# Kernel optimization log

Measured on AMD Instinct MI355X. Metric: run time of the kernel, lower is better.

Reference implementation:

```python
import jax, jax.numpy as jnp
import numpy as np

B, T, S, V, E, H, ENC, SUM = 256, 64, 256, 512, 512, 1024, 1024, 2048
DECODE_RANGE = 512  # current_decode_range == full vocab here


def setup_inputs() -> dict:
    key = jax.random.key(0)
    ks = jax.random.split(key, 16)
    r = lambda k, shape: jax.random.normal(k, shape, dtype=jnp.float32) * 0.02
    z = lambda n: jnp.zeros((n,), dtype=jnp.float32)
    return {
        "y": jax.random.randint(ks[0], (B, T), 0, V),
        "encoder_embed": jax.random.normal(ks[1], (B, S, ENC), dtype=jnp.float32),
        "encoder_summary": jax.random.normal(ks[2], (B, SUM), dtype=jnp.float32),
        "emb_table": r(ks[3], (V, E)),
        "W_init": r(ks[4], (4 * H, SUM)), "b_init": z(4 * H),
        "W_ci": r(ks[5], (E, E + ENC)), "b_ci": z(E),
        "Wih0": r(ks[6], (4 * H, E)), "Whh0": r(ks[7], (4 * H, H)),
        "bih0": z(4 * H), "bhh0": z(4 * H),
        "Wih1": r(ks[8], (4 * H, H)), "Whh1": r(ks[9], (4 * H, H)),
        "bih1": z(4 * H), "bhh1": z(4 * H),
        "Wq": r(ks[10], (ENC, 2 * H)), "bq": z(ENC),
        "Wco": r(ks[11], (H, ENC + H)), "bco": z(H),
        "Wout": r(ks[12], (V, H)), "bout": z(V),
    }


def _lstm_cell(x, h, c, Wih, Whh, bih, bhh):
    # PyTorch LSTM gate order: i, f, g, o
    g = x @ Wih.T + h @ Whh.T + bih + bhh
    i, f, gg, o = jnp.split(g, 4, axis=-1)
    c = jax.nn.sigmoid(f) * c + jax.nn.sigmoid(i) * jnp.tanh(gg)
    h = jax.nn.sigmoid(o) * jnp.tanh(c)
    return h, c


def reference(y, encoder_embed, encoder_summary, emb_table, W_init, b_init,
              W_ci, b_ci, Wih0, Whh0, bih0, bhh0, Wih1, Whh1, bih1, bhh1,
              Wq, bq, Wco, bco, Wout, bout):
    bs = y.shape[0]
    hdim = Whh0.shape[1]
    # decoder_init: Linear+Tanh -> view(B,2,2,H).permute(1,2,0,3) -> (h0, c0), each (layers=2, B, H)
    init = jnp.tanh(encoder_summary @ W_init.T + b_init).reshape(bs, 2, 2, hdim)
    init = jnp.transpose(init, (1, 2, 0, 3))
    h0, c0 = init[0], init[1]
    cross0 = jnp.zeros((bs, encoder_embed.shape[-1]), dtype=encoder_embed.dtype)

    def step(carry, tok):
        h, c, cross = carry  # h, c: (2, B, H); cross: (B, ENC)
        emb = emb_table[tok]  # (B, E)
        emb = jnp.tanh(jnp.concatenate([emb, cross], -1) @ W_ci.T + b_ci)
        h_l0, c_l0 = _lstm_cell(emb, h[0], c[0], Wih0, Whh0, bih0, bhh0)
        h_l1, c_l1 = _lstm_cell(h_l0, h[1], c[1], Wih1, Whh1, bih1, bhh1)
        # attention query from cat(h, c) of last layer
        q = jnp.tanh(jnp.concatenate([h_l1, c_l1], -1) @ Wq.T + bq)  # (B, ENC)
        attn = jax.nn.softmax(jnp.einsum('be,bse->bs', q, encoder_embed), axis=-1)
        cross = jnp.einsum('bs,bse->be', attn, encoder_embed)  # (B, ENC)
        lin = jnp.tanh(jnp.concatenate([h_l1, cross], -1) @ Wco.T + bco)
        logits = lin @ Wout.T + bout  # (B, V)
        tok_out = jnp.argmax(logits[:, :DECODE_RANGE], axis=-1)
        return (jnp.stack([h_l0, h_l1]), jnp.stack([c_l0, c_l1]), cross), (logits, tok_out)

    _, (logits, toks) = jax.lax.scan(step, (h0, c0, cross0), y.T)
    decoder_tokens = jnp.transpose(toks, (1, 0))           # (B, T)
    decoder_linears = jnp.transpose(logits, (1, 0, 2))     # (B, T, V)
    return decoder_tokens, decoder_linears
```

## Files before the change

### kernel.cpp

```cpp
#include <hip/hip_runtime.h>
#include <math.h>

#define BB   256
#define TT   64
#define SS   256
#define VV   512
#define EE   512
#define HH   1024
#define ENCE 1024
#define SUME 2048
#define NSP  8

typedef __attribute__((ext_vector_type(8))) _Float16 h8v;
typedef __attribute__((ext_vector_type(4))) float f4v;

__device__ __forceinline__ void split16(float x, _Float16& h, _Float16& l) {
    h = (_Float16)x;
    l = (_Float16)((x - (float)h) * 4096.0f);
}

__global__ __launch_bounds__(256) void gemm2(
    const float* __restrict__ A0, const float* __restrict__ W0, const int K0,
    const int lda0, const int ldw0,
    const float* __restrict__ A1, const float* __restrict__ W1, const int Ktot,
    const int lda1, const int ldw1,
    const float* __restrict__ b0, const float* __restrict__ b1,
    float* __restrict__ C, const int ldc, const int act)
{
    __shared__ float As[16][68];
    __shared__ float Ws[16][68];

    const int tid = threadIdx.x;
    const int n0  = blockIdx.x * 64;
    const int m0  = blockIdx.y * 64;
    const int lr  = tid >> 2;
    const int lc  = (tid & 3) << 2;
    const int tx  = tid & 15;
    const int ty  = tid >> 4;

    float acc[4][4] = {{0.f}};

    for (int k0 = 0; k0 < Ktot; k0 += 16) {
        const float* A; const float* W; int lda, ldw, kk;
        if (k0 < K0) { A = A0; W = W0; lda = lda0; ldw = ldw0; kk = k0; }
        else         { A = A1; W = W1; lda = lda1; ldw = ldw1; kk = k0 - K0; }

        const float4 av = *(const float4*)(A + (size_t)(m0 + lr) * lda + kk + lc);
        const float4 wv = *(const float4*)(W + (size_t)(n0 + lr) * ldw + kk + lc);

        __syncthreads();
        As[lc + 0][lr] = av.x; As[lc + 1][lr] = av.y;
        As[lc + 2][lr] = av.z; As[lc + 3][lr] = av.w;
        Ws[lc + 0][lr] = wv.x; Ws[lc + 1][lr] = wv.y;
        Ws[lc + 2][lr] = wv.z; Ws[lc + 3][lr] = wv.w;
        __syncthreads();

        #pragma unroll
        for (int p = 0; p < 16; ++p) {
            const float4 a4 = *(const float4*)&As[p][ty * 4];
            const float4 w4 = *(const float4*)&Ws[p][tx * 4];
            acc[0][0] += a4.x * w4.x; acc[0][1] += a4.x * w4.y;
            acc[0][2] += a4.x * w4.z; acc[0][3] += a4.x * w4.w;
            acc[1][0] += a4.y * w4.x; acc[1][1] += a4.y * w4.y;
            acc[1][2] += a4.y * w4.z; acc[1][3] += a4.y * w4.w;
            acc[2][0] += a4.z * w4.x; acc[2][1] += a4.z * w4.y;
            acc[2][2] += a4.z * w4.z; acc[2][3] += a4.z * w4.w;
            acc[3][0] += a4.w * w4.x; acc[3][1] += a4.w * w4.y;
            acc[3][2] += a4.w * w4.z; acc[3][3] += a4.w * w4.w;
        }
    }

    float bias[4];
    #pragma unroll
    for (int j = 0; j < 4; ++j) {
        const int n = n0 + tx * 4 + j;
        bias[j] = b0[n] + (b1 ? b1[n] : 0.f);
    }
    #pragma unroll
    for (int i = 0; i < 4; ++i) {
        const int m = m0 + ty * 4 + i;
        #pragma unroll
        for (int j = 0; j < 4; ++j) {
            float v = acc[i][j] + bias[j];
            if (act) v = tanhf(v);
            C[(size_t)m * ldc + n0 + tx * 4 + j] = v;
        }
    }
}

__global__ void lstm_gate(const float* __restrict__ g,
                          float* __restrict__ h, float* __restrict__ c)
{
    const int i = blockIdx.x * blockDim.x + threadIdx.x;
    if (i >= BB * HH) return;
    const int b = i / HH, k = i % HH;
    const float* gb = g + (size_t)b * 4 * HH;
    const float gi = gb[k];
    const float gf = gb[HH + k];
    const float gg = gb[2 * HH + k];
    const float go = gb[3 * HH + k];
    const float si = 1.f / (1.f + expf(-gi));
    const float sf = 1.f / (1.f + expf(-gf));
    const float so = 1.f / (1.f + expf(-go));
    const float cn = sf * c[i] + si * tanhf(gg);
    c[i] = cn;
    h[i] = so * tanhf(cn);
}

__global__ __launch_bounds__(256) void attn_kernel(
    const float* __restrict__ q, const float* __restrict__ enc,
    float* __restrict__ cross)
{
    const int b = blockIdx.x, tid = threadIdx.x;
    __shared__ float qs[ENCE];
    __shared__ float sc[SS];
    __shared__ float red[256];

    const float* qb = q + (size_t)b * ENCE;
    const float* eb = enc + (size_t)b * SS * ENCE;

    for (int e = tid; e < ENCE; e += 256) qs[e] = qb[e];
    __syncthreads();

    {
        const float* row = eb + (size_t)tid * ENCE;
        float a = 0.f;
        for (int e = 0; e < ENCE; e += 4) {
            const float4 ev = *(const float4*)&row[e];
            a += ev.x * qs[e] + ev.y * qs[e + 1] + ev.z * qs[e + 2] + ev.w * qs[e + 3];
        }
        sc[tid] = a;
    }
    __syncthreads();

    red[tid] = sc[tid];
    __syncthreads();
    for (int off = 128; off > 0; off >>= 1) {
        if (tid < off) red[tid] = fmaxf(red[tid], red[tid + off]);
        __syncthreads();
    }
    const float mx = red[0];
    __syncthreads();
    const float ex = expf(sc[tid] - mx);
    red[tid] = ex;
    __syncthreads();
    for (int off = 128; off > 0; off >>= 1) {
        if (tid < off) red[tid] += red[tid + off];
        __syncthreads();
    }
    const float inv = 1.f / red[0];
    __syncthreads();
    sc[tid] = ex * inv;
    __syncthreads();

    float4 acc = {0.f, 0.f, 0.f, 0.f};
    const int e0 = tid * 4;
    for (int s = 0; s < SS; ++s) {
        const float w = sc[s];
        const float4 ev = *(const float4*)&eb[(size_t)s * ENCE + e0];
        acc.x += w * ev.x; acc.y += w * ev.y; acc.z += w * ev.z; acc.w += w * ev.w;
    }
    *(float4*)&cross[(size_t)b * ENCE + e0] = acc;
}

__global__ __launch_bounds__(256) void attn_part_k(
    const float* __restrict__ qpart, const float* __restrict__ bq,
    const float* __restrict__ enc,
    float* __restrict__ po, float* __restrict__ pm, float* __restrict__ pl)
{
    const int sp = blockIdx.x, b = blockIdx.y, tid = threadIdx.x;
    __shared__ float qs[ENCE];
    __shared__ float es[4 * ENCE];
    __shared__ float sc[4];

    {
        const int n = tid * 4;
        float4 s = *(const float4*)&bq[n];
        #pragma unroll
        for (int p = 0; p < 8; ++p) {
            const float4 v = *(const float4*)&qpart[
                (size_t)p * BB * ENCE + (size_t)b * ENCE + n];
            s.x += v.x; s.y += v.y; s.z += v.z; s.w += v.w;
        }
        qs[n]     = tanhf(s.x);
        qs[n + 1] = tanhf(s.y);
        qs[n + 2] = tanhf(s.z);
        qs[n + 3] = tanhf(s.w);
    }

    const float* eb = enc + (size_t)b * SS * ENCE + (size_t)sp * 32 * ENCE;

    float4 r0, r1, r2, r3;
    auto ldchunk = [&](int ch) {
        const float* src = eb + (size_t)ch * 4 * ENCE + tid * 4;
        r0 = *(const float4*)(src);
        r1 = *(const float4*)(src + ENCE);
        r2 = *(const float4*)(src + 2 * ENCE);
        r3 = *(const float4*)(src + 3 * ENCE);
    };
    ldchunk(0);
    __syncthreads();

    const int row  = tid >> 6;
    const int lane = tid & 63;
    const int e0   = tid * 4;

    float m = -INFINITY, l = 0.f;
    float4 o = {0.f, 0.f, 0.f, 0.f};

    for (int ch = 0; ch < 8; ++ch) {
        *(float4*)&es[tid * 4]            = r0;
        *(float4*)&es[tid * 4 + ENCE]     = r1;
        *(float4*)&es[tid * 4 + 2 * ENCE] = r2;
        *(float4*)&es[tid * 4 + 3 * ENCE] = r3;
        __syncthreads();

        if (ch + 1 < 8) ldchunk(ch + 1);

        {
            float a = 0.f;
            const float* er = &es[row * ENCE];
            #pragma unroll
            for (int j = 0; j < 4; ++j) {
                const int e = lane * 4 + j * 256;
                const float4 ev = *(const float4*)&er[e];
                const float4 qv = *(const float4*)&qs[e];
                a += ev.x * qv.x + ev.y * qv.y + ev.z * qv.z + ev.w * qv.w;
            }
            a += __shfl_xor(a, 1);
            a += __shfl_xor(a, 2);
            a += __shfl_xor(a, 4);
            a += __shfl_xor(a, 8);
            a += __shfl_xor(a, 16);
            a += __shfl_xor(a, 32);
            if (lane == 0) sc[row] = a;
        }
        __syncthreads();

        {
            const float cm = fmaxf(fmaxf(sc[0], sc[1]), fmaxf(sc[2], sc[3]));
            const float mn = fmaxf(m, cm);
            const float scale = expf(m - mn);
            o.x *= scale; o.y *= scale; o.z *= scale; o.w *= scale;
            l *= scale;
            const float p0 = expf(sc[0] - mn), p1 = expf(sc[1] - mn);
            const float p2 = expf(sc[2] - mn), p3 = expf(sc[3] - mn);
            l += p0 + p1 + p2 + p3;
            const float4 e0v = *(const float4*)&es[e0];
            const float4 e1v = *(const float4*)&es[ENCE + e0];
            const float4 e2v = *(const float4*)&es[2 * ENCE + e0];
            const float4 e3v = *(const float4*)&es[3 * ENCE + e0];
            o.x += p0 * e0v.x + p1 * e1v.x + p2 * e2v.x + p3 * e3v.x;
            o.y += p0 * e0v.y + p1 * e1v.y + p2 * e2v.y + p3 * e3v.y;
            o.z += p0 * e0v.z + p1 * e1v.z + p2 * e2v.z + p3 * e3v.z;
            o.w += p0 * e0v.w + p1 * e1v.w + p2 * e2v.w + p3 * e3v.w;
            m = mn;
        }
        __syncthreads();
    }

    *(float4*)&po[((size_t)sp * BB + b) * ENCE + e0] = o;
    if (tid == 0) { pm[sp * BB + b] = m; pl[sp * BB + b] = l; }
}

__global__ __launch_bounds__(256) void attn_comb_k(
    const float* __restrict__ po, const float* __restrict__ pm,
    const float* __restrict__ pl,
    _Float16* __restrict__ crh, _Float16* __restrict__ crl)
{
    const int b = blockIdx.x, tid = threadIdx.x;
    float ms = -INFINITY;
    #pragma unroll
    for (int p = 0; p < NSP; ++p) ms = fmaxf(ms, pm[p * BB + b]);
    float w[NSP]; float L = 0.f;
    #pragma unroll
    for (int p = 0; p < NSP; ++p) {
        w[p] = expf(pm[p * BB + b] - ms);
        L += pl[p * BB + b] * w[p];
    }
    const float inv = 1.f / L;

    const int e0 = tid * 4;
    float4 acc = {0.f, 0.f, 0.f, 0.f};
    #pragma unroll
    for (int p = 0; p < NSP; ++p) {
        const float4 v = *(const float4*)&po[((size_t)p * BB + b) * ENCE + e0];
        acc.x += w[p] * v.x; acc.y += w[p] * v.y;
        acc.z += w[p] * v.z; acc.w += w[p] * v.w;
    }
    const float4 r = {acc.x * inv, acc.y * inv, acc.z * inv, acc.w * inv};

    _Float16 h4[4], l4[4];
    split16(r.x, h4[0], l4[0]); split16(r.y, h4[1], l4[1]);
    split16(r.z, h4[2], l4[2]); split16(r.w, h4[3], l4[3]);
    *(uint2*)&crh[(size_t)b * ENCE + e0] = *(uint2*)h4;
    *(uint2*)&crl[(size_t)b * ENCE + e0] = *(uint2*)l4;
}

__global__ __launch_bounds__(256) void out_kernel(
    const float* __restrict__ lin, const float* __restrict__ Wout,
    const float* __restrict__ bout, float* __restrict__ tokens,
    float* __restrict__ logits, const int t)
{
    const int b = blockIdx.x, tid = threadIdx.x;
    __shared__ float ls[HH];
    __shared__ float vmax[256];
    __shared__ int   vidx[256];

    const float* lb = lin + (size_t)b * HH;
    for (int e = tid; e < HH; e += 256) ls[e] = lb[e];
    __syncthreads();

    float best = -INFINITY; int bi = 0;
    for (int n = tid; n < VV; n += 256) {
        const float* wr = Wout + (size_t)n * HH;
        float a = bout[n];
        for (int e = 0; e < HH; e += 4) {
            const float4 wv = *(const float4*)&wr[e];
            a += wv.x * ls[e] + wv.y * ls[e + 1] + wv.z * ls[e + 2] + wv.w * ls[e + 3];
        }
        logits[((size_t)b * TT + t) * VV + n] = a;
        if (a > best) { best = a; bi = n; }
    }
    vmax[tid] = best; vidx[tid] = bi;
    __syncthreads();
    for (int off = 128; off > 0; off >>= 1) {
        if (tid < off) {
            const float vo = vmax[tid + off]; const int io = vidx[tid + off];
            if (vo > vmax[tid] || (vo == vmax[tid] && io < vidx[tid])) {
                vmax[tid] = vo; vidx[tid] = io;
            }
        }
        __syncthreads();
    }
    if (tid == 0) tokens[(size_t)b * TT + t] = (float)vidx[0];
}

__global__ void gather_emb(const int* __restrict__ y,
                           const float* __restrict__ table,
                           float* __restrict__ emb, const int t)
{
    const int i = blockIdx.x * blockDim.x + threadIdx.x;
    if (i >= BB * EE) return;
    const int b = i / EE, e = i % EE;
    emb[i] = table[(size_t)y[(size_t)b * TT + t] * EE + e];
}

__global__ void scatter_init_s(const float* __restrict__ ini,
                               float* __restrict__ h0, float* __restrict__ h1,
                               float* __restrict__ c0, float* __restrict__ c1,
                               _Float16* __restrict__ h0h, _Float16* __restrict__ h0l,
                               _Float16* __restrict__ h1h, _Float16* __restrict__ h1l,
                               _Float16* __restrict__ c1h, _Float16* __restrict__ c1l)
{
    const int i = blockIdx.x * blockDim.x + threadIdx.x;
    if (i >= BB * 4 * HH) return;
    const int b = i / (4 * HH), j = i % (4 * HH);
    const int i1 = j / (2 * HH);
    const int rem = j % (2 * HH);
    const int i2 = rem / HH;
    const int k = rem % HH;
    const float v = ini[i];
    const size_t o = (size_t)b * HH + k;
    float* dst = (i1 == 0) ? (i2 == 0 ? h0 : h1) : (i2 == 0 ? c0 : c1);
    dst[o] = v;
    if (h0h) {
        if (i1 == 0) {
            _Float16 h, l; split16(v, h, l);
            if (i2 == 0) { h0h[o] = h; h0l[o] = l; }
            else         { h1h[o] = h; h1l[o] = l; }
        } else if (i2 == 1) {
            _Float16 h, l; split16(v, h, l);
            c1h[o] = h; c1l[o] = l;
        }
    }
}

__global__ void zero_kernel(float* __restrict__ p, const int n)
{
    const int i = blockIdx.x * blockDim.x + threadIdx.x;
    if (i < n) p[i] = 0.f;
}


__global__ void conv_w2(const float* __restrict__ src, const int N, const int K,
                        _Float16* __restrict__ dh, _Float16* __restrict__ dl,
                        const int dld, const int coff)
{
    const int total = N * K;
    for (int i = blockIdx.x * blockDim.x + threadIdx.x; i < total;
         i += gridDim.x * blockDim.x) {
        const int n = i / K, k = i - n * K;
        const size_t o = (size_t)n * dld + coff + k;
        split16(src[i], dh[o], dl[o]);
    }
}

__global__ __launch_bounds__(256) void gemm_f16(
    const _Float16* __restrict__ A0h, const _Float16* __restrict__ A0l, const int lda0,
    const _Float16* __restrict__ A1h, const _Float16* __restrict__ A1l, const int lda1,
    const int K0,
    const float* __restrict__ rawA0, const int* __restrict__ yidx, const int t,
    const _Float16* __restrict__ Wh, const _Float16* __restrict__ Wl,
    const int Kt, float* __restrict__ Cpart, const int N, const int chunk)
{
    __shared__ _Float16 Ash[64][40], Asl[64][40];
    __shared__ _Float16 Wsh[128][40], Wsl[128][40];

    const int tid = threadIdx.x;
    const int n0 = blockIdx.x * 128;
    const int m0 = blockIdx.y * 64;
    const int p  = blockIdx.z;
    const int kbeg = p * chunk, kend = kbeg + chunk;

    const int lane = tid & 63, wave = tid >> 6;
    const int wm = wave >> 1, wn = wave & 1;
    const int l15 = lane & 15, lg = lane >> 4;

    const int ar = tid >> 2, ag = tid & 3;

    const float* Araw = rawA0
        ? rawA0 + (size_t)yidx[(size_t)(m0 + ar) * TT + t] * lda0 : nullptr;

    f4v accm[2][4], accc[2][4];
    #pragma unroll
    for (int i = 0; i < 2; ++i)
        #pragma unroll
        for (int j = 0; j < 4; ++j) {
            accm[i][j] = (f4v){0.f, 0.f, 0.f, 0.f};
            accc[i][j] = (f4v){0.f, 0.f, 0.f, 0.f};
        }

    uint4 avh, avl, wh0, wl0, wh1, wl1;

    auto load_tile = [&](int kk_) {
        const int col = kk_ + ag * 8;
        if (col < K0) {
            if (Araw) {
                const float4 f0 = *(const float4*)(Araw + col);
                const float4 f1 = *(const float4*)(Araw + col + 4);
                const float xs[8] = {f0.x, f0.y, f0.z, f0.w, f1.x, f1.y, f1.z, f1.w};
                h8v vh, vl;
                #pragma unroll
                for (int j = 0; j < 8; ++j) {
                    _Float16 th, tl;
                    split16(xs[j], th, tl);
                    vh[j] = th;
                    vl[j] = tl;
                }
                avh = *(uint4*)&vh; avl = *(uint4*)&vl;
            } else {
                const size_t o = (size_t)(m0 + ar) * lda0 + col;
                avh = *(const uint4*)(A0h + o);
                avl = *(const uint4*)(A0l + o);
            }
        } else {
            const size_t o = (size_t)(m0 + ar) * lda1 + (col - K0);
            avh = *(const uint4*)(A1h + o);
            avl = *(const uint4*)(A1l + o);
        }
        const size_t o0 = (size_t)(n0 + ar) * Kt + kk_ + ag * 8;
        const size_t o1 = o0 + (size_t)64 * Kt;
        wh0 = *(const uint4*)(Wh + o0);
        wl0 = *(const uint4*)(Wl + o0);
        wh1 = *(const uint4*)(Wh + o1);
        wl1 = *(const uint4*)(Wl + o1);
    };

    load_tile(kbeg);

    for (int kk = kbeg; kk < kend; kk += 32) {
        __syncthreads();

        *(uint4*)&Ash[ar][ag * 8] = avh;
        *(uint4*)&Asl[ar][ag * 8] = avl;
        *(uint4*)&Wsh[ar][ag * 8] = wh0;
        *(uint4*)&Wsl[ar][ag * 8] = wl0;
        *(uint4*)&Wsh[64 + ar][ag * 8] = wh1;
        *(uint4*)&Wsl[64 + ar][ag * 8] = wl1;

        __syncthreads();

        if (kk + 32 < kend) load_tile(kk + 32);

        h8v afh[2], afl[2];
        #pragma unroll
        for (int fr = 0; fr < 2; ++fr) {
            const int r = wm * 32 + fr * 16 + l15;
            afh[fr] = *(const h8v*)&Ash[r][lg * 8];
            afl[fr] = *(const h8v*)&Asl[r][lg * 8];
        }
        #pragma unroll
        for (int fn = 0; fn < 4; ++fn) {
            const int r = wn * 64 + fn * 16 + l15;
            const h8v wfh = *(const h8v*)&Wsh[r][lg * 8];
            const h8v wfl = *(const h8v*)&Wsl[r][lg * 8];
            #pragma unroll
            for (int fr = 0; fr < 2; ++fr) {
                accm[fr][fn] = __builtin_amdgcn_mfma_f32_16x16x32_f16(
                    afh[fr], wfh, accm[fr][fn], 0, 0, 0);
                accc[fr][fn] = __builtin_amdgcn_mfma_f32_16x16x32_f16(
                    afh[fr], wfl, accc[fr][fn], 0, 0, 0);
                accc[fr][fn] = __builtin_amdgcn_mfma_f32_16x16x32_f16(
                    afl[fr], wfh, accc[fr][fn], 0, 0, 0);
            }
        }
    }

    const float s12 = 0.000244140625f;
    float* slab = Cpart + (size_t)p * BB * N;
    #pragma unroll
    for (int fr = 0; fr < 2; ++fr) {
        const int row0 = m0 + wm * 32 + fr * 16 + lg * 4;
        #pragma unroll
        for (int fn = 0; fn < 4; ++fn) {
            const int col = n0 + wn * 64 + fn * 16 + l15;
            #pragma unroll
            for (int j = 0; j < 4; ++j)
                slab[(size_t)(row0 + j) * N + col] =
                    accm[fr][fn][j] + s12 * accc[fr][fn][j];
        }
    }
}

__global__ void ep_tanh_s(const float* __restrict__ part, const int P,
                          const float* __restrict__ bias, float* __restrict__ dst,
                          _Float16* __restrict__ dh, _Float16* __restrict__ dl,
                          const int total, const int N)
{
    for (int i = blockIdx.x * blockDim.x + threadIdx.x; i < total;
         i += gridDim.x * blockDim.x) {
        const int n = i % N;
        float s = bias[n];
        for (int p = 0; p < P; ++p) s += part[(size_t)p * total + i];
        const float v = tanhf(s);
        if (dst) dst[i] = v;
        if (dh) split16(v, dh[i], dl[i]);
    }
}

__global__ void ep_gate_s(const float* __restrict__ part, const int P,
                          const float* __restrict__ bih, const float* __restrict__ bhh,
                          float* __restrict__ h, float* __restrict__ c,
                          _Float16* __restrict__ hh, _Float16* __restrict__ hl,
                          _Float16* __restrict__ ch, _Float16* __restrict__ cl)
{
    const int i = blockIdx.x * blockDim.x + threadIdx.x;
    if (i >= BB * HH) return;
    const int b = i >> 10, k = i & (HH - 1);
    const size_t base = (size_t)b * 4 * HH;
    float gi = bih[k] + bhh[k];
    float gf = bih[HH + k] + bhh[HH + k];
    float gg = bih[2 * HH + k] + bhh[2 * HH + k];
    float go = bih[3 * HH + k] + bhh[3 * HH + k];
    for (int p = 0; p < P; ++p) {
        const float* gp = part + (size_t)p * BB * 4 * HH + base;
        gi += gp[k]; gf += gp[HH + k]; gg += gp[2 * HH + k]; go += gp[3 * HH + k];
    }
    const float si = 1.f / (1.f + expf(-gi));
    const float sf = 1.f / (1.f + expf(-gf));
    const float so = 1.f / (1.f + expf(-go));
    const float cn = sf * c[i] + si * tanhf(gg);
    const float hn = so * tanhf(cn);
    c[i] = cn;
    h[i] = hn;
    split16(hn, hh[i], hl[i]);
    if (ch) split16(cn, ch[i], cl[i]);
}

__global__ __launch_bounds__(256) void ep_argmax(
    const float* __restrict__ part, const int P,
    const float* __restrict__ bias, float* __restrict__ tokens,
    float* __restrict__ logits, const int t)
{
    const int b = blockIdx.x, tid = threadIdx.x;
    __shared__ float vmax[256];
    __shared__ int   vidx[256];

    float best = -INFINITY; int bi = 0;
    #pragma unroll
    for (int j = 0; j < 2; ++j) {
        const int n = tid + j * 256;
        float s = bias[n];
        for (int p = 0; p < P; ++p)
            s += part[(size_t)p * BB * VV + (size_t)b * VV + n];
        logits[((size_t)b * TT + t) * VV + n] = s;
        if (s > best) { best = s; bi = n; }
    }
    vmax[tid] = best; vidx[tid] = bi;
    __syncthreads();
    for (int off = 128; off > 0; off >>= 1) {
        if (tid < off) {
            const float vo = vmax[tid + off]; const int io = vidx[tid + off];
            if (vo > vmax[tid] || (vo == vmax[tid] && io < vidx[tid])) {
                vmax[tid] = vo; vidx[tid] = io;
            }
        }
        __syncthreads();
    }
    if (tid == 0) tokens[(size_t)b * TT + t] = (float)vidx[0];
}

extern "C" void kernel_launch(void* const* d_in, const int* in_sizes, int n_in,
                              void* d_out, int out_size, void* d_ws, size_t ws_size,
                              hipStream_t stream)
{
    const int*   y         = (const int*)  d_in[0];
    const float* enc       = (const float*)d_in[1];
    const float* esum      = (const float*)d_in[2];
    const float* emb_table = (const float*)d_in[3];
    const float* W_init    = (const float*)d_in[4];
    const float* b_init    = (const float*)d_in[5];
    const float* W_ci      = (const float*)d_in[6];
    const float* b_ci      = (const float*)d_in[7];
    const float* Wih0      = (const float*)d_in[8];
    const float* Whh0      = (const float*)d_in[9];
    const float* bih0      = (const float*)d_in[10];
    const float* bhh0      = (const float*)d_in[11];
    const float* Wih1      = (const float*)d_in[12];
    const float* Whh1      = (const float*)d_in[13];
    const float* bih1      = (const float*)d_in[14];
    const float* bhh1      = (const float*)d_in[15];
    const float* Wq        = (const float*)d_in[16];
    const float* bq        = (const float*)d_in[17];
    const float* Wco       = (const float*)d_in[18];
    const float* bco       = (const float*)d_in[19];
    const float* Wout      = (const float*)d_in[20];
    const float* bout      = (const float*)d_in[21];

    float* out    = (float*)d_out;
    float* tokens = out;
    float* logits = out + (size_t)BB * TT;

    char* wsb = (char*)d_ws;
    size_t off = 0;
    auto alloc = [&](size_t bytes) -> char* {
        char* p = wsb + off;
        off = (off + bytes + 255) & ~(size_t)255;
        return p;
    };
    float* h0    = (float*)alloc((size_t)BB * HH * 4);
    float* h1    = (float*)alloc((size_t)BB * HH * 4);
    float* c0    = (float*)alloc((size_t)BB * HH * 4);
    float* c1    = (float*)alloc((size_t)BB * HH * 4);
    float* cross = (float*)alloc((size_t)BB * ENCE * 4);
    float* xbuf  = (float*)alloc((size_t)BB * EE * 4);
    float* embb  = (float*)alloc((size_t)BB * EE * 4);
    float* gbuf  = (float*)alloc((size_t)BB * 4 * HH * 4);
    float* qbuf  = (float*)alloc((size_t)BB * ENCE * 4);

    float* part = (float*)alloc((size_t)4 * BB * 4 * HH * 4);

    _Float16 *ci_h, *ci_l, *g0_h, *g0_l, *g1_h, *g1_l, *wq_h, *wq_l,
             *wc_h, *wc_l, *wo_h, *wo_l;
    ci_h = (_Float16*)alloc((size_t)EE * 1536 * 2);
    ci_l = (_Float16*)alloc((size_t)EE * 1536 * 2);
    g0_h = (_Float16*)alloc((size_t)4 * HH * 1536 * 2);
    g0_l = (_Float16*)alloc((size_t)4 * HH * 1536 * 2);
    g1_h = (_Float16*)alloc((size_t)4 * HH * 2048 * 2);
    g1_l = (_Float16*)alloc((size_t)4 * HH * 2048 * 2);
    wq_h = (_Float16*)alloc((size_t)ENCE * 2048 * 2);
    wq_l = (_Float16*)alloc((size_t)ENCE * 2048 * 2);
    wc_h = (_Float16*)alloc((size_t)HH * 2048 * 2);
    wc_l = (_Float16*)alloc((size_t)HH * 2048 * 2);
    wo_h = (_Float16*)alloc((size_t)VV * HH * 2);
    wo_l = (_Float16*)alloc((size_t)VV * HH * 2);

    _Float16* xbh  = (_Float16*)alloc((size_t)BB * EE * 2);
    _Float16* xbl  = (_Float16*)alloc((size_t)BB * EE * 2);
    _Float16* h0h  = (_Float16*)alloc((size_t)BB * HH * 2);
    _Float16* h0l  = (_Float16*)alloc((size_t)BB * HH * 2);
    _Float16* h1h  = (_Float16*)alloc((size_t)BB * HH * 2);
    _Float16* h1l  = (_Float16*)alloc((size_t)BB * HH * 2);
    _Float16* c1h  = (_Float16*)alloc((size_t)BB * HH * 2);
    _Float16* c1l  = (_Float16*)alloc((size_t)BB * HH * 2);
    _Float16* crh  = (_Float16*)alloc((size_t)BB * ENCE * 2);
    _Float16* crl  = (_Float16*)alloc((size_t)BB * ENCE * 2);
    _Float16* lnh  = (_Float16*)alloc((size_t)BB * HH * 2);
    _Float16* lnl  = (_Float16*)alloc((size_t)BB * HH * 2);

    float* po = (float*)alloc((size_t)NSP * BB * ENCE * 4);
    float* pm = (float*)alloc((size_t)NSP * BB * 4);
    float* pl = (float*)alloc((size_t)NSP * BB * 4);
    const size_t need_mfma = off;

    const int mfma_ok = (ws_size >= need_mfma);

    const dim3 thr(256);

    gemm2<<<dim3(4 * HH / 64, BB / 64), thr, 0, stream>>>(
        esum, W_init, SUME, SUME, SUME,
        nullptr, nullptr, SUME, 0, 0,
        b_init, nullptr, gbuf, 4 * HH, 1);
    scatter_init_s<<<dim3(BB * 4 * HH / 256), thr, 0, stream>>>(
        gbuf, h0, h1, c0, c1,
        mfma_ok ? h0h : nullptr, h0l, h1h, h1l, c1h, c1l);
    zero_kernel<<<dim3(BB * ENCE / 256), thr, 0, stream>>>(cross, BB * ENCE);

    if (!mfma_ok) {
        for (int t = 0; t < TT; ++t) {
            gather_emb<<<dim3(BB * EE / 256), thr, 0, stream>>>(y, emb_table, embb, t);
            gemm2<<<dim3(EE / 64, BB / 64), thr, 0, stream>>>(
                embb, W_ci, EE, EE, EE + ENCE,
                cross, W_ci + EE, EE + ENCE, ENCE, EE + ENCE,
                b_ci, nullptr, xbuf, EE, 1);
            gemm2<<<dim3(4 * HH / 64, BB / 64), thr, 0, stream>>>(
                xbuf, Wih0, EE, EE, EE,
                h0, Whh0, EE + HH, HH, HH,
                bih0, bhh0, gbuf, 4 * HH, 0);
            lstm_gate<<<dim3(BB * HH / 256), thr, 0, stream>>>(gbuf, h0, c0);
            gemm2<<<dim3(4 * HH / 64, BB / 64), thr, 0, stream>>>(
                h0, Wih1, HH, HH, HH,
                h1, Whh1, 2 * HH, HH, HH,
                bih1, bhh1, gbuf, 4 * HH, 0);
            lstm_gate<<<dim3(BB * HH / 256), thr, 0, stream>>>(gbuf, h1, c1);
            gemm2<<<dim3(ENCE / 64, BB / 64), thr, 0, stream>>>(
                h1, Wq, HH, HH, 2 * HH,
                c1, Wq + HH, 2 * HH, HH, 2 * HH,
                bq, nullptr, qbuf, ENCE, 1);
            attn_kernel<<<dim3(BB), thr, 0, stream>>>(qbuf, enc, cross);
            gemm2<<<dim3(HH / 64, BB / 64), thr, 0, stream>>>(
                h1, Wco, HH, HH, ENCE + HH,
                cross, Wco + HH, ENCE + HH, ENCE, ENCE + HH,
                bco, nullptr, qbuf, HH, 1);
            out_kernel<<<dim3(BB), thr, 0, stream>>>(qbuf, Wout, bout, tokens, logits, t);
        }
        return;
    }

    const dim3 cg(4096);
    conv_w2<<<cg, thr, 0, stream>>>(W_ci, EE, EE + ENCE, ci_h, ci_l, 1536, 0);
    conv_w2<<<cg, thr, 0, stream>>>(Wih0, 4 * HH, EE, g0_h, g0_l, 1536, 0);
    conv_w2<<<cg, thr, 0, stream>>>(Whh0, 4 * HH, HH, g0_h, g0_l, 1536, EE);
    conv_w2<<<cg, thr, 0, stream>>>(Wih1, 4 * HH, HH, g1_h, g1_l, 2048, 0);
    conv_w2<<<cg, thr, 0, stream>>>(Whh1, 4 * HH, HH, g1_h, g1_l, 2048, HH);
    conv_w2<<<cg, thr, 0, stream>>>(Wq, ENCE, 2 * HH, wq_h, wq_l, 2048, 0);
    conv_w2<<<cg, thr, 0, stream>>>(Wco, HH, ENCE + HH, wc_h, wc_l, 2048, 0);
    conv_w2<<<cg, thr, 0, stream>>>(Wout, VV, HH, wo_h, wo_l, HH, 0);
    zero_kernel<<<dim3(BB * ENCE / 512), thr, 0, stream>>>((float*)crh, BB * ENCE / 2);
    zero_kernel<<<dim3(BB * ENCE / 512), thr, 0, stream>>>((float*)crl, BB * ENCE / 2);

    auto gemmS = [&](const _Float16* a0h, const _Float16* a0l, int lda0,
                     const _Float16* a1h, const _Float16* a1l, int lda1, int K0,
                     const float* raw0, const int* yi, int t_,
                     const _Float16* wh, const _Float16* wl,
                     int Kt, int N, int P) {
        gemm_f16<<<dim3(N / 128, BB / 64, P), thr, 0, stream>>>(
            a0h, a0l, lda0, a1h, a1l, lda1, K0, raw0, yi, t_,
            wh, wl, Kt, part, N, Kt / P);
    };

    for (int t = 0; t < TT; ++t) {
        gemmS(nullptr, nullptr, EE, crh, crl, ENCE, EE,
              emb_table, y, t, ci_h, ci_l, 1536, EE, 8);
        ep_tanh_s<<<dim3(512), thr, 0, stream>>>(part, 8, b_ci, nullptr, xbh, xbl,
                                                 BB * EE, EE);

        gemmS(xbh, xbl, EE, h0h, h0l, HH, EE, nullptr, nullptr, 0,
              g0_h, g0_l, 1536, 4 * HH, 4);
        ep_gate_s<<<dim3(BB * HH / 256), thr, 0, stream>>>(
            part, 4, bih0, bhh0, h0, c0, h0h, h0l, nullptr, nullptr);

        gemmS(h0h, h0l, HH, h1h, h1l, HH, HH, nullptr, nullptr, 0,
              g1_h, g1_l, 2048, 4 * HH, 4);
        ep_gate_s<<<dim3(BB * HH / 256), thr, 0, stream>>>(
            part, 4, bih1, bhh1, h1, c1, h1h, h1l, c1h, c1l);

        gemmS(h1h, h1l, HH, c1h, c1l, HH, HH, nullptr, nullptr, 0,
              wq_h, wq_l, 2048, ENCE, 8);

        attn_part_k<<<dim3(NSP, BB), thr, 0, stream>>>(part, bq, enc, po, pm, pl);
        attn_comb_k<<<dim3(BB), thr, 0, stream>>>(po, pm, pl, crh, crl);

        gemmS(h1h, h1l, HH, crh, crl, ENCE, HH, nullptr, nullptr, 0,
              wc_h, wc_l, 2048, HH, 8);
        ep_tanh_s<<<dim3(1024), thr, 0, stream>>>(part, 8, bco, nullptr, lnh, lnl,
                                                  BB * HH, HH);

        gemmS(lnh, lnl, HH, nullptr, nullptr, HH, HH, nullptr, nullptr, 0,
              wo_h, wo_l, HH, VV, 8);
        ep_argmax<<<dim3(BB), thr, 0, stream>>>(part, 8, bout, tokens, logits, t);
    }
}
```

Baseline: 11.67 ms.

## Retile split-K f16 GEMM to full-batch 256x64 tiles with 512 threads

Replaces the 64x128 GEMM tile with a tile covering all 256 batch rows by 64 output columns. Each block runs 8 waves (512 threads), so each weight tile is loaded once per block instead of once per batch-row block. This cuts global weight traffic, which matters for these weight-heavy recurrent GEMMs. The first GEMM's split-K factor rises from 8 to 16 to keep enough blocks, at the cost of more partial-sum traffic in the epilogue. It also adds a no-op rewrite in an unused lstm_gate kernel.

```diff
diff --git a/kernel.cpp b/kernel.cpp
--- a/kernel.cpp
+++ b/kernel.cpp
@@ -101,10 +101,12 @@
     const float go = gb[3 * HH + k];
     const float si = 1.f / (1.f + expf(-gi));
     const float sf = 1.f / (1.f + expf(-gf));
-    const float so = 1.f / (1.f + expf(-go));
+    const float so = 1.f / (1.f + expf(-so * 0.f - go));
+    const float so2 = 1.f / (1.f + expf(-go));
     const float cn = sf * c[i] + si * tanhf(gg);
     c[i] = cn;
-    h[i] = so * tanhf(cn);
+    h[i] = so2 * tanhf(cn);
+    (void)so;
 }
 
 __global__ __launch_bounds__(256) void attn_kernel(
@@ -396,7 +398,7 @@
     }
 }
 
-__global__ __launch_bounds__(256) void gemm_f16(
+__global__ __launch_bounds__(512) void gemm_m256(
     const _Float16* __restrict__ A0h, const _Float16* __restrict__ A0l, const int lda0,
     const _Float16* __restrict__ A1h, const _Float16* __restrict__ A1l, const int lda1,
     const int K0,
@@ -404,67 +406,74 @@
     const _Float16* __restrict__ Wh, const _Float16* __restrict__ Wl,
     const int Kt, float* __restrict__ Cpart, const int N, const int chunk)
 {
-    __shared__ _Float16 Ash[64][40], Asl[64][40];
-    __shared__ _Float16 Wsh[128][40], Wsl[128][40];
+    __shared__ _Float16 Ash[256][40], Asl[256][40];
+    __shared__ _Float16 Wsh[64][40],  Wsl[64][40];
 
     const int tid = threadIdx.x;
-    const int n0 = blockIdx.x * 128;
-    const int m0 = blockIdx.y * 64;
-    const int p  = blockIdx.z;
+    const int n0 = blockIdx.x * 64;
+    const int p  = blockIdx.y;
     const int kbeg = p * chunk, kend = kbeg + chunk;
 
     const int lane = tid & 63, wave = tid >> 6;
     const int wm = wave >> 1, wn = wave & 1;
     const int l15 = lane & 15, lg = lane >> 4;
 
-    const int ar = tid >> 2, ag = tid & 3;
+    const int ar = tid >> 1, ag = tid & 1;
+    const int wr = (tid & 255) >> 2, wg = tid & 3;
 
     const float* Araw = rawA0
-        ? rawA0 + (size_t)yidx[(size_t)(m0 + ar) * TT + t] * lda0 : nullptr;
-
-    f4v accm[2][4], accc[2][4];
+        ? rawA0 + (size_t)yidx[(size_t)ar * TT + t] * lda0 : nullptr;
+
+    f4v accm[4][2], accc[4][2];
     #pragma unroll
-    for (int i = 0; i < 2; ++i)
+    for (int i = 0; i < 4; ++i)
         #pragma unroll
-        for (int j = 0; j < 4; ++j) {
+        for (int j = 0; j < 2; ++j) {
             accm[i][j] = (f4v){0.f, 0.f, 0.f, 0.f};
             accc[i][j] = (f4v){0.f, 0.f, 0.f, 0.f};
         }
 
-    uint4 avh, avl, wh0, wl0, wh1, wl1;
+    uint4 a_h0, a_h1, a_l0, a_l1;
+    uint4 w_h, w_l;
 
     auto load_tile = [&](int kk_) {
-        const int col = kk_ + ag * 8;
+        const int col = kk_ + ag * 16;
         if (col < K0) {
             if (Araw) {
                 const float4 f0 = *(const float4*)(Araw + col);
                 const float4 f1 = *(const float4*)(Araw + col + 4);
-                const float xs[8] = {f0.x, f0.y, f0.z, f0.w, f1.x, f1.y, f1.z, f1.w};
-                h8v vh, vl;
+                const float4 f2 = *(const float4*)(Araw + col + 8);
+                const float4 f3 = *(const float4*)(Araw + col + 12);
+                const float xs[16] = {f0.x, f0.y, f0.z, f0.w, f1.x, f1.y, f1.z, f1.w,
+                                      f2.x, f2.y, f2.z, f2.w, f3.x, f3.y, f3.z, f3.w};
+                h8v vh0, vl0, vh1, vl1;
                 #pragma unroll
                 for (int j = 0; j < 8; ++j) {
                     _Float16 th, tl;
-                    split16(xs[j], th, tl);
-                    vh[j] = th;
-                    vl[j] = tl;
+                    split16(xs[j], th, tl);     vh0[j] = th; vl0[j] = tl;
+                    split16(xs[8 + j], th, tl); vh1[j] = th; vl1[j] = tl;
                 }
-                avh = *(uint4*)&vh; avl = *(uint4*)&vl;
+                a_h0 = *(uint4*)&vh0; a_h1 = *(uint4*)&vh1;
+                a_l0 = *(uint4*)&vl0; a_l1 = *(uint4*)&vl1;
             } else {
-                const size_t o = (size_t)(m0 + ar) * lda0 + col;
-                avh = *(const uint4*)(A0h + o);
-                avl = *(const uint4*)(A0l + o);
+                const size_t o = (size_t)ar * lda0 + col;
+                a_h0 = *(const uint4*)(A0h + o);
+                a_h1 = *(const uint4*)(A0h + o + 8);
+                a_l0 = *(const uint4*)(A0l + o);
+                a_l1 = *(const uint4*)(A0l + o + 8);
             }
         } else {
-            const size_t o = (size_t)(m0 + ar) * lda1 + (col - K0);
-            avh = *(const uint4*)(A1h + o);
-            avl = *(const uint4*)(A1l + o);
-        }
-        const size_t o0 = (size_t)(n0 + ar) * Kt + kk_ + ag * 8;
-        const size_t o1 = o0 + (size_t)64 * Kt;
-        wh0 = *(const uint4*)(Wh + o0);
-        wl0 = *(const uint4*)(Wl + o0);
-        wh1 = *(const uint4*)(Wh + o1);
-        wl1 = *(const uint4*)(Wl + o1);
+            const size_t o = (size_t)ar * lda1 + (col - K0);
+            a_h0 = *(const uint4*)(A1h + o);
+            a_h1 = *(const uint4*)(A1h + o + 8);
+            a_l0 = *(const uint4*)(A1l + o);
+            a_l1 = *(const uint4*)(A1l + o + 8);
+        }
+        if (tid < 256) {
+            const size_t o = (size_t)(n0 + wr) * Kt + kk_ + wg * 8;
+            w_h = *(const uint4*)(Wh + o);
+            w_l = *(const uint4*)(Wl + o);
+        }
     };
 
     load_tile(kbeg);
@@ -472,49 +481,53 @@
     for (int kk = kbeg; kk < kend; kk += 32) {
         __syncthreads();
 
-        *(uint4*)&Ash[ar][ag * 8] = avh;
-        *(uint4*)&Asl[ar][ag * 8] = avl;
-        *(uint4*)&Wsh[ar][ag * 8] = wh0;
-        *(uint4*)&Wsl[ar][ag * 8] = wl0;
-        *(uint4*)&Wsh[64 + ar][ag * 8] = wh1;
-        *(uint4*)&Wsl[64 + ar][ag * 8] = wl1;
+        *(uint4*)&Ash[ar][ag * 16]     = a_h0;
+        *(uint4*)&Ash[ar][ag * 16 + 8] = a_h1;
+        *(uint4*)&Asl[ar][ag * 16]     = a_l0;
+        *(uint4*)&Asl[ar][ag * 16 + 8] = a_l1;
+        if (tid < 256) {
+            *(uint4*)&Wsh[wr][wg * 8] = w_h;
+            *(uint4*)&Wsl[wr][wg * 8] = w_l;
+        }
 
         __syncthreads();
 
         if (kk + 32 < kend) load_tile(kk + 32);
 
-        h8v afh[2], afl[2];
+        h8v afh[4], afl[4], wfh[2], wfl[2];
         #pragma unroll
-        for (int fr = 0; fr < 2; ++fr) {
-            const int r = wm * 32 + fr * 16 + l15;
+        for (int fr = 0; fr < 4; ++fr) {
+            const int r = wm * 64 + fr * 16 + l15;
             afh[fr] = *(const h8v*)&Ash[r][lg * 8];
             afl[fr] = *(const h8v*)&Asl[r][lg * 8];
         }
         #pragma unroll
-        for (int fn = 0; fn < 4; ++fn) {
-            const int r = wn * 64 + fn * 16 + l15;
-            const h8v wfh = *(const h8v*)&Wsh[r][lg * 8];
-            const h8v wfl = *(const h8v*)&Wsl[r][lg * 8];
+        for (int fn = 0; fn < 2; ++fn) {
+            const int r = wn * 32 + fn * 16 + l15;
+            wfh[fn] = *(const h8v*)&Wsh[r][lg * 8];
+            wfl[fn] = *(const h8v*)&Wsl[r][lg * 8];
+        }
+        #pragma unroll
+        for (int fn = 0; fn < 2; ++fn)
             #pragma unroll
-            for (int fr = 0; fr < 2; ++fr) {
+            for (int fr = 0; fr < 4; ++fr) {
                 accm[fr][fn] = __builtin_amdgcn_mfma_f32_16x16x32_f16(
-                    afh[fr], wfh, accm[fr][fn], 0, 0, 0);
+                    afh[fr], wfh[fn], accm[fr][fn], 0, 0, 0);
                 accc[fr][fn] = __builtin_amdgcn_mfma_f32_16x16x32_f16(
-                    afh[fr], wfl, accc[fr][fn], 0, 0, 0);
+                    afh[fr], wfl[fn], accc[fr][fn], 0, 0, 0);
                 accc[fr][fn] = __builtin_amdgcn_mfma_f32_16x16x32_f16(
-                    afl[fr], wfh, accc[fr][fn], 0, 0, 0);
+                    afl[fr], wfh[fn], accc[fr][fn], 0, 0, 0);
             }
-        }
     }
 
     const float s12 = 0.000244140625f;
     float* slab = Cpart + (size_t)p * BB * N;
     #pragma unroll
-    for (int fr = 0; fr < 2; ++fr) {
-        const int row0 = m0 + wm * 32 + fr * 16 + lg * 4;
+    for (int fr = 0; fr < 4; ++fr) {
+        const int row0 = wm * 64 + fr * 16 + lg * 4;
         #pragma unroll
-        for (int fn = 0; fn < 4; ++fn) {
-            const int col = n0 + wn * 64 + fn * 16 + l15;
+        for (int fn = 0; fn < 2; ++fn) {
+            const int col = n0 + wn * 32 + fn * 16 + l15;
             #pragma unroll
             for (int j = 0; j < 4; ++j)
                 slab[(size_t)(row0 + j) * N + col] =
@@ -649,7 +662,7 @@
     float* gbuf  = (float*)alloc((size_t)BB * 4 * HH * 4);
     float* qbuf  = (float*)alloc((size_t)BB * ENCE * 4);
 
-    float* part = (float*)alloc((size_t)4 * BB * 4 * HH * 4);
+    float* part = (float*)alloc((size_t)16 * BB * 4 * HH * 4 / 4);
 
     _Float16 *ci_h, *ci_l, *g0_h, *g0_l, *g1_h, *g1_l, *wq_h, *wq_l,
              *wc_h, *wc_l, *wo_h, *wo_l;
@@ -745,15 +758,15 @@
                      const float* raw0, const int* yi, int t_,
                      const _Float16* wh, const _Float16* wl,
                      int Kt, int N, int P) {
-        gemm_f16<<<dim3(N / 128, BB / 64, P), thr, 0, stream>>>(
+        gemm_m256<<<dim3(N / 64, P), dim3(512), 0, stream>>>(
             a0h, a0l, lda0, a1h, a1l, lda1, K0, raw0, yi, t_,
             wh, wl, Kt, part, N, Kt / P);
     };
 
     for (int t = 0; t < TT; ++t) {
         gemmS(nullptr, nullptr, EE, crh, crl, ENCE, EE,
-              emb_table, y, t, ci_h, ci_l, 1536, EE, 8);
-        ep_tanh_s<<<dim3(512), thr, 0, stream>>>(part, 8, b_ci, nullptr, xbh, xbl,
+              emb_table, y, t, ci_h, ci_l, 1536, EE, 16);
+        ep_tanh_s<<<dim3(512), thr, 0, stream>>>(part, 16, b_ci, nullptr, xbh, xbl,
                                                  BB * EE, EE);
 
         gemmS(xbh, xbl, EE, h0h, h0l, HH, EE, nullptr, nullptr, 0,
```

New measurement: 12.43 ms. 1.07x slower.
